# Optimization experiments

Measured on AMD Instinct MI355X. Metric: run time of the kernel, lower is better.

Reference implementation:

```python
import jax, jax.numpy as jnp
import numpy as np

ALPHA = 0.25
GAMMA = 2.0
EPS = 1e-8
W_CLASS = 2.0
W_BBOX = 5.0
W_GIOU = 2.0
B, Q, T, C = 64, 900, 300, 80


def setup_inputs() -> dict:
    key = jax.random.key(0)
    k1, k2, k3, k4 = jax.random.split(key, 4)
    pred_logits = jax.random.normal(k1, (B, Q, C), dtype=jnp.float32)
    pred_boxes = jax.random.uniform(k2, (B, Q, 4), dtype=jnp.float32)  # cxcywh in (0,1)
    tgt_labels = jax.random.randint(k3, (B, T), 0, C, dtype=jnp.int64)
    tgt_boxes = jax.random.uniform(k4, (B, T, 4), dtype=jnp.float32)
    return {"pred_logits": pred_logits, "pred_boxes": pred_boxes,
            "tgt_labels": tgt_labels, "tgt_boxes": tgt_boxes}


def box_cxcywh_to_xyxy(b):
    cx, cy, w, h = b[..., 0], b[..., 1], b[..., 2], b[..., 3]
    return jnp.stack([cx - 0.5 * w, cy - 0.5 * h, cx + 0.5 * w, cy + 0.5 * h], axis=-1)


def pairwise_giou(boxes1, boxes2):
    # boxes1: [B,Q,4] xyxy, boxes2: [B,T,4] xyxy -> [B,Q,T]
    area1 = (boxes1[..., 2] - boxes1[..., 0]) * (boxes1[..., 3] - boxes1[..., 1])
    area2 = (boxes2[..., 2] - boxes2[..., 0]) * (boxes2[..., 3] - boxes2[..., 1])
    lt = jnp.maximum(boxes1[:, :, None, :2], boxes2[:, None, :, :2])
    rb = jnp.minimum(boxes1[:, :, None, 2:], boxes2[:, None, :, 2:])
    wh = jnp.clip(rb - lt, 0.0)
    inter = wh[..., 0] * wh[..., 1]
    union = area1[:, :, None] + area2[:, None, :] - inter
    iou = inter / union
    lt_c = jnp.minimum(boxes1[:, :, None, :2], boxes2[:, None, :, :2])
    rb_c = jnp.maximum(boxes1[:, :, None, 2:], boxes2[:, None, :, 2:])
    wh_c = jnp.clip(rb_c - lt_c, 0.0)
    area_c = wh_c[..., 0] * wh_c[..., 1]
    return iou - (area_c - union) / area_c


def reference(pred_logits, pred_boxes, tgt_labels, tgt_boxes):
    # Batched cost matrix of HungarianMatcher (use_focal_loss=True).
    prob = jax.nn.sigmoid(pred_logits)  # [B,Q,C]
    idx = jnp.broadcast_to(tgt_labels[:, None, :], (prob.shape[0], prob.shape[1], tgt_labels.shape[1]))
    p = jnp.take_along_axis(prob, idx.astype(jnp.int32), axis=2)  # [B,Q,T]
    neg_cost = (1.0 - ALPHA) * p ** GAMMA * (-jnp.log(1.0 - p + EPS))
    pos_cost = ALPHA * (1.0 - p) ** GAMMA * (-jnp.log(p + EPS))
    cost_class = pos_cost - neg_cost
    cost_bbox = jnp.abs(pred_boxes[:, :, None, :] - tgt_boxes[:, None, :, :]).sum(-1)
    cost_giou = -pairwise_giou(box_cxcywh_to_xyxy(pred_boxes), box_cxcywh_to_xyxy(tgt_boxes))
    cost = W_BBOX * cost_bbox + W_CLASS * cost_class + W_GIOU * cost_giou
    return jnp.nan_to_num(cost, nan=1.0, posinf=1e6, neginf=-1e6)
```

## Files before the change

### kernel.cpp

```cpp
#include <hip/hip_runtime.h>


constexpr int B = 64, Q = 900, T = 300, C = 80;
constexpr int QTILE = 12;
constexpr int BLOCK = 256;
constexpr int NTQ   = 3;
constexpr int NQ    = QTILE / NTQ;
constexpr float ALPHA = 0.25f;

__device__ __forceinline__ float fast_rcp(float x) {
    return __builtin_amdgcn_rcpf(x);
}

__device__ __forceinline__ float focal2(float x) {
    float t  = __expf(-x);
    float p  = fast_rcp(1.0f + t);
    float L  = __logf(1.0f + t);
    float xL = x + L;
    float omp = t * p;
    float pos = ALPHA * omp * omp * L;
    float neg = (1.0f - ALPHA) * p * p * xL;
    return fmaf(2.0f, pos - neg, 2.0f);
}

__global__ __launch_bounds__(BLOCK) void matcher_cost_kernel(
    const float* __restrict__ logits,
    const float* __restrict__ pboxes,
    const int*   __restrict__ tlabels,
    const float* __restrict__ tboxes,
    float* __restrict__ out)
{
    __shared__ float  s_cls[QTILE * C];
    __shared__ float4 s_pB[QTILE];

    const int bid = blockIdx.x;
    const int b   = bid / (Q / QTILE);
    const int q0  = (bid % (Q / QTILE)) * QTILE;
    const int tid = threadIdx.x;

    if (tid < QTILE) {
        float4 bx = *(const float4*)(pboxes + ((size_t)b * Q + q0 + tid) * 4);
        s_pB[tid] = make_float4(bx.x - 0.5f * bx.z, bx.y - 0.5f * bx.w,
                                bx.x + 0.5f * bx.z, bx.y + 0.5f * bx.w);
    }
    {
        const float* lg = logits + ((size_t)b * Q + q0) * C;
        for (int i = tid; i < QTILE * C; i += BLOCK)
            s_cls[i] = focal2(lg[i]);
    }

    const int tq = tid / 75;
    const int tt = tid - tq * 75;
    const bool active = (tid < NTQ * 75);

    float Tx0[4], Ty0[4], Tx1[4], Ty1[4];
    int lab[4] = {0, 0, 0, 0};
    if (active) {
        const float4* tbp = (const float4*)(tboxes + ((size_t)b * T + tt * 4) * 4);
        int4 lb = *(const int4*)(tlabels + (size_t)b * T + tt * 4);
        lab[0] = lb.x; lab[1] = lb.y; lab[2] = lb.z; lab[3] = lb.w;
        #pragma unroll
        for (int k = 0; k < 4; ++k) {
            float4 bx = tbp[k];
            Tx0[k] = bx.x - 0.5f * bx.z; Ty0[k] = bx.y - 0.5f * bx.w;
            Tx1[k] = bx.x + 0.5f * bx.z; Ty1[k] = bx.y + 0.5f * bx.w;
        }
    }

    __syncthreads();

    if (!active) return;

    const float* cls0 = s_cls + tq * C;
    float* op = out + ((size_t)b * Q + q0 + tq) * T + tt * 4;

    #pragma unroll
    for (int j = 0; j < NQ; ++j) {
        float4 pB = s_pB[tq + NTQ * j];
        float pw = pB.z - pB.x, ph = pB.w - pB.y;
        float pa = pw * ph;
        const float* clsj = cls0 + j * NTQ * C;

        float cls_k[4] = { clsj[lab[0]], clsj[lab[1]], clsj[lab[2]], clsj[lab[3]] };

        float4 res;
        #pragma unroll
        for (int k = 0; k < 4; ++k) {
            float dx0 = pB.x - Tx0[k], dx1 = pB.z - Tx1[k];
            float dy0 = pB.y - Ty0[k], dy1 = pB.w - Ty1[k];

            float tw = Tx1[k] - Tx0[k], th = Ty1[k] - Ty0[k];
            float ta = tw * th;

            float wi = fminf(pB.z, Tx1[k]) - fmaxf(pB.x, Tx0[k]);
            float hi = fminf(pB.w, Ty1[k]) - fmaxf(pB.y, Ty0[k]);
            float iw = fmaxf(wi, 0.0f), ih = fmaxf(hi, 0.0f);
            float inter = iw * ih;
            float uni = (pa + ta) - inter;
            float cw  = (pw + tw) - wi;
            float ch  = (ph + th) - hi;
            float ca  = cw * ch;

            float cb = fabsf(dx1 - dx0) + fabsf(dy1 - dy0);
            cb = fmaf(0.5f, fabsf(dx0 + dx1), cb);
            cb = fmaf(0.5f, fabsf(dy0 + dy1), cb);

            float num = fmaf(uni, uni, inter * ca);
            float r   = fast_rcp(uni * ca);
            float c   = fmaf(5.0f, cb, cls_k[k]);
            c = fmaf(num * r, -2.0f, c);

            if (c != c) c = 1.0f;

            (&res.x)[k] = c;
        }
        *(float4*)(op + (size_t)(NTQ * j) * T) = res;
    }
}

extern "C" void kernel_launch(void* const* d_in, const int* in_sizes, int n_in,
                              void* d_out, int out_size, void* d_ws, size_t ws_size,
                              hipStream_t stream) {
    const float* logits  = (const float*)d_in[0];
    const float* pboxes  = (const float*)d_in[1];
    const int*   tlabels = (const int*)  d_in[2];
    const float* tboxes  = (const float*)d_in[3];
    float* out = (float*)d_out;

    dim3 grid(B * (Q / QTILE));
    dim3 block(BLOCK);
    matcher_cost_kernel<<<grid, block, 0, stream>>>(logits, pboxes, tlabels, tboxes, out);
}
```

Measured before the change: 32.14 us.

## Retile to 18 queries per 320-thread block with 2 targets per thread

Result: no change. 31.63 us (-1.6%).

```diff
diff --git a/kernel.cpp b/kernel.cpp
--- a/kernel.cpp
+++ b/kernel.cpp
@@ -2,9 +2,9 @@
 
 
 constexpr int B = 64, Q = 900, T = 300, C = 80;
-constexpr int QTILE = 12;
-constexpr int BLOCK = 256;
-constexpr int NTQ   = 3;
+constexpr int QTILE = 18;
+constexpr int BLOCK = 320;
+constexpr int NTQ   = 2;
 constexpr int NQ    = QTILE / NTQ;
 constexpr float ALPHA = 0.25f;
 
@@ -49,21 +49,24 @@
             s_cls[i] = focal2(lg[i]);
     }
 
-    const int tq = tid / 75;
-    const int tt = tid - tq * 75;
-    const bool active = (tid < NTQ * 75);
+    const int tq = tid / 150;
+    const int tt = tid - tq * 150;
+    const bool active = (tid < NTQ * 150);
 
-    float Tx0[4], Ty0[4], Tx1[4], Ty1[4];
-    int lab[4] = {0, 0, 0, 0};
+    float Tx0[2], Ty0[2], Tx1[2], Ty1[2];
+    float tw[2], th[2], ta[2], tsx[2], tsy[2];
+    int lab[2] = {0, 0};
     if (active) {
-        const float4* tbp = (const float4*)(tboxes + ((size_t)b * T + tt * 4) * 4);
-        int4 lb = *(const int4*)(tlabels + (size_t)b * T + tt * 4);
-        lab[0] = lb.x; lab[1] = lb.y; lab[2] = lb.z; lab[3] = lb.w;
+        const float4* tbp = (const float4*)(tboxes + ((size_t)b * T + tt * 2) * 4);
+        int2 lb = *(const int2*)(tlabels + (size_t)b * T + tt * 2);
+        lab[0] = lb.x; lab[1] = lb.y;
         #pragma unroll
-        for (int k = 0; k < 4; ++k) {
+        for (int k = 0; k < 2; ++k) {
             float4 bx = tbp[k];
             Tx0[k] = bx.x - 0.5f * bx.z; Ty0[k] = bx.y - 0.5f * bx.w;
             Tx1[k] = bx.x + 0.5f * bx.z; Ty1[k] = bx.y + 0.5f * bx.w;
+            tw[k]  = bx.z;  th[k] = bx.w;  ta[k] = bx.z * bx.w;
+            tsx[k] = Tx0[k] + Tx1[k];      tsy[k] = Ty0[k] + Ty1[k];
         }
     }
 
@@ -72,38 +75,33 @@
     if (!active) return;
 
     const float* cls0 = s_cls + tq * C;
-    float* op = out + ((size_t)b * Q + q0 + tq) * T + tt * 4;
+    float* op = out + ((size_t)b * Q + q0 + tq) * T + tt * 2;
 
     #pragma unroll
     for (int j = 0; j < NQ; ++j) {
         float4 pB = s_pB[tq + NTQ * j];
-        float pw = pB.z - pB.x, ph = pB.w - pB.y;
-        float pa = pw * ph;
+        float pw  = pB.z - pB.x, ph = pB.w - pB.y;
+        float pa  = pw * ph;
+        float psx = pB.x + pB.z, psy = pB.y + pB.w;
         const float* clsj = cls0 + j * NTQ * C;
 
-        float cls_k[4] = { clsj[lab[0]], clsj[lab[1]], clsj[lab[2]], clsj[lab[3]] };
+        float cls_k[2] = { clsj[lab[0]], clsj[lab[1]] };
 
-        float4 res;
+        float2 res;
         #pragma unroll
-        for (int k = 0; k < 4; ++k) {
-            float dx0 = pB.x - Tx0[k], dx1 = pB.z - Tx1[k];
-            float dy0 = pB.y - Ty0[k], dy1 = pB.w - Ty1[k];
-
-            float tw = Tx1[k] - Tx0[k], th = Ty1[k] - Ty0[k];
-            float ta = tw * th;
-
+        for (int k = 0; k < 2; ++k) {
             float wi = fminf(pB.z, Tx1[k]) - fmaxf(pB.x, Tx0[k]);
             float hi = fminf(pB.w, Ty1[k]) - fmaxf(pB.y, Ty0[k]);
             float iw = fmaxf(wi, 0.0f), ih = fmaxf(hi, 0.0f);
             float inter = iw * ih;
-            float uni = (pa + ta) - inter;
-            float cw  = (pw + tw) - wi;
-            float ch  = (ph + th) - hi;
+            float uni = (pa + ta[k]) - inter;
+            float cw  = (pw + tw[k]) - wi;
+            float ch  = (ph + th[k]) - hi;
             float ca  = cw * ch;
 
-            float cb = fabsf(dx1 - dx0) + fabsf(dy1 - dy0);
-            cb = fmaf(0.5f, fabsf(dx0 + dx1), cb);
-            cb = fmaf(0.5f, fabsf(dy0 + dy1), cb);
+            float cb = fabsf(pw - tw[k]) + fabsf(ph - th[k]);
+            float cs = fabsf(psx - tsx[k]) + fabsf(psy - tsy[k]);
+            cb = fmaf(0.5f, cs, cb);
 
             float num = fmaf(uni, uni, inter * ca);
             float r   = fast_rcp(uni * ca);
@@ -114,7 +112,7 @@
 
             (&res.x)[k] = c;
         }
-        *(float4*)(op + (size_t)(NTQ * j) * T) = res;
+        *(float2*)(op + (size_t)(NTQ * j) * T) = res;
     }
 }
 
```
